# Kernel tuning notes

Measured on AMD Instinct MI355X. Metric: run time of the kernel, lower is better.

The kernel has to match this reference:

```python
import jax, jax.numpy as jnp
import numpy as np

TEMPERATURE = 0.5
BATCH_SIZE = 4096
EPS = 1e-8  # torch.nn.CosineSimilarity default eps


def setup_inputs() -> dict:
    key = jax.random.key(0)
    k1, k2 = jax.random.split(key)
    z1 = jax.random.normal(k1, (BATCH_SIZE, 256), dtype=jnp.float32)
    z2 = jax.random.normal(k2, (BATCH_SIZE, 256), dtype=jnp.float32)
    return {"z1": z1, "z2": z2}


def reference(z1, z2):
    B = z1.shape[0]
    N = 2 * B
    reps = jnp.concatenate([z1, z2], axis=0)  # [N, D]
    # Cosine similarity (torch clamps each norm to eps before dividing)
    norms = jnp.maximum(jnp.linalg.norm(reps, axis=1, keepdims=True), EPS)
    z = reps / norms
    sim = z @ z.T  # [N, N] cosine similarity matrix

    # positives: diagonals at offsets +B and -B (they are identical by symmetry,
    # but keep the original concat order: [diag(+B), diag(-B)])
    l_pos = jnp.diagonal(sim, offset=B)
    r_pos = jnp.diagonal(sim, offset=-B)
    positives = jnp.concatenate([l_pos, r_pos])  # [N]

    inv_t = 1.0 / TEMPERATURE
    pos_logit = positives * inv_t  # logits[:, 0]

    # negatives are all off-diagonal entries of each row (the positive pair is
    # thus present twice in the logits, faithful to the original). CE with
    # label 0 => loss_i = logsumexp(logits_i) - logits_i[0].
    neg_logits = jnp.where(jnp.eye(N, dtype=bool), -jnp.inf, sim * inv_t)
    lse = jnp.logaddexp(pos_logit, jax.scipy.special.logsumexp(neg_logits, axis=1))
    loss = jnp.sum(lse - pos_logit) / N
    return loss
```

## Files before the change

### kernel.cpp

```cpp
#include <hip/hip_runtime.h>
#include <hip/hip_bf16.h>
#include <cstdint>
#include <cstddef>
#include <math.h>

#define BSZ   4096
#define NROW  8192
#define DIM   256
#define INV_T 2.0f
#define EPS_N 1e-8f
#define CE    2.8853900817779268f
#define NTILE 2080

typedef __attribute__((ext_vector_type(8))) short bf16x8;
typedef __attribute__((ext_vector_type(4))) float f32x4;

struct TileOrder {
    unsigned short idx[NTILE];
    constexpr TileOrder() : idx{} {
        int pga[28] = {}, pgb[28] = {};
        int np = 0;
        for (int a = 0; a < 8; ++a)
            for (int b = a + 1; b < 8; ++b) { pga[np] = a; pgb[np] = b; ++np; }
        int seq[8][260] = {};
        for (int x = 0; x < 8; ++x) {
            int n = 0;
            for (int i = 0; i < 8; ++i)
                for (int j = i; j < 8; ++j)
                    seq[x][n++] = ((8 * x + i) << 8) | (8 * x + j);
            for (int p = 0; p < 3; ++p) {
                const int ga = pga[3 * x + p], gb = pgb[3 * x + p];
                for (int i = 0; i < 8; ++i)
                    for (int j = 0; j < 8; ++j)
                        seq[x][n++] = ((8 * ga + i) << 8) | (8 * gb + j);
            }
            const int pi = 24 + x / 2;
            const int ga = pga[pi], gb = pgb[pi];
            const int i0 = (x & 1) ? 4 : 0;
            for (int i = i0; i < i0 + 4; ++i)
                for (int j = 0; j < 8; ++j)
                    seq[x][n++] = ((8 * ga + i) << 8) | (8 * gb + j);
        }
        for (int l = 0; l < NTILE; ++l)
            idx[l] = (unsigned short)seq[l % 8][l / 8];
    }
};
__device__ constexpr TileOrder TO{};

__device__ __forceinline__ unsigned short f2bf(float x) {
    __hip_bfloat16 h = __float2bfloat16(x);
    return __builtin_bit_cast(unsigned short, h);
}
__device__ __forceinline__ float bf2f(unsigned short u) {
    __hip_bfloat16 h = __builtin_bit_cast(__hip_bfloat16, u);
    return __bfloat162float(h);
}

__device__ __forceinline__ void load_lds16(const void* g, void* l) {
    __builtin_amdgcn_global_load_lds(
        (const __attribute__((address_space(1))) void*)g,
        (__attribute__((address_space(3))) void*)l,
        16, 0, 0);
}

__global__ __launch_bounds__(256)
void nt_normalize(const float* __restrict__ z1,
                  const float* __restrict__ z2,
                  __hip_bfloat16* __restrict__ zn,
                  float* __restrict__ rowsum,
                  float* __restrict__ sii) {
    const int wave = threadIdx.x >> 6;
    const int lane = threadIdx.x & 63;
    const int row  = blockIdx.x * 4 + wave;
    const float* src = (row < BSZ) ? (z1 + (size_t)row * DIM)
                                   : (z2 + (size_t)(row - BSZ) * DIM);
    const float4 v = ((const float4*)src)[lane];
    float ss = v.x * v.x + v.y * v.y + v.z * v.z + v.w * v.w;
    #pragma unroll
    for (int off = 32; off; off >>= 1) ss += __shfl_xor(ss, off);
    const float rinv = 1.0f / fmaxf(sqrtf(ss), EPS_N);
    ushort4 o;
    o.x = f2bf(v.x * rinv);
    o.y = f2bf(v.y * rinv);
    o.z = f2bf(v.z * rinv);
    o.w = f2bf(v.w * rinv);
    ((ushort4*)(zn + (size_t)row * DIM))[lane] = o;
    float bx = bf2f(o.x), by = bf2f(o.y), bz = bf2f(o.z), bw = bf2f(o.w);
    float s2 = bx * bx + by * by + bz * bz + bw * bw;
    #pragma unroll
    for (int off = 32; off; off >>= 1) s2 += __shfl_xor(s2, off);
    if (lane == 0) { sii[row] = s2; rowsum[row] = 0.0f; }
}

__global__ __launch_bounds__(256)
void nt_gram(const __hip_bfloat16* __restrict__ zn,
             float* __restrict__ rowsum,
             float* __restrict__ pos) {
    const int code = TO.idx[blockIdx.x];
    const int bi = code >> 8, bj = code & 255;

    __shared__ __hip_bfloat16 As[128 * 64];
    __shared__ __hip_bfloat16 Bs[128 * 64];

    const int t    = threadIdx.x;
    const int lane = t & 63;
    const int wave = t >> 6;
    const int wrow = (wave >> 1) * 64;
    const int wcol = (wave & 1) * 64;
    const int q    = lane >> 4;
    const int r16  = lane & 15;
    const int sw   = r16 & 7;

    f32x4 acc[4][4] = {};

    const __hip_bfloat16* Ag = zn + (size_t)bi * 128 * DIM;
    const __hip_bfloat16* Bg = zn + (size_t)bj * 128 * DIM;

    const int srow = t >> 3;
    const int sc   = (t & 7) ^ (srow & 7);

    for (int k0 = 0; k0 < DIM; k0 += 64) {
        #pragma unroll
        for (int p = 0; p < 4; ++p) {
            const int row = p * 32 + srow;
            load_lds16(Ag + (size_t)row * DIM + k0 + sc * 8,
                       (char*)As + p * 4096 + t * 16);
            load_lds16(Bg + (size_t)row * DIM + k0 + sc * 8,
                       (char*)Bs + p * 4096 + t * 16);
        }
        __syncthreads();

        #pragma unroll
        for (int kk = 0; kk < 64; kk += 32) {
            const int cc = (kk >> 3) + q;
            const int cpos = (cc ^ sw) << 4;
            bf16x8 af[4], bfr[4];
            #pragma unroll
            for (int mi = 0; mi < 4; ++mi) {
                const int m = wrow + mi * 16 + r16;
                af[mi] = *(const bf16x8*)((const char*)As + m * 128 + cpos);
            }
            #pragma unroll
            for (int ni = 0; ni < 4; ++ni) {
                const int n = wcol + ni * 16 + r16;
                bfr[ni] = *(const bf16x8*)((const char*)Bs + n * 128 + cpos);
            }
            #pragma unroll
            for (int mi = 0; mi < 4; ++mi)
                #pragma unroll
                for (int ni = 0; ni < 4; ++ni)
                    acc[mi][ni] = __builtin_amdgcn_mfma_f32_16x16x32_bf16(
                        af[mi], bfr[ni], acc[mi][ni], 0, 0, 0);
        }
        __syncthreads();
    }

    const int c = lane & 15;
    float colp[4] = {0.f, 0.f, 0.f, 0.f};

    #pragma unroll
    for (int mi = 0; mi < 4; ++mi) {
        #pragma unroll
        for (int r = 0; r < 4; ++r) {
            float s = 0.f;
            #pragma unroll
            for (int ni = 0; ni < 4; ++ni) {
                const float e = exp2f(acc[mi][ni][r] * CE);
                s += e;
                colp[ni] += e;
            }
            s += __shfl_xor(s, 1);
            s += __shfl_xor(s, 2);
            s += __shfl_xor(s, 4);
            s += __shfl_xor(s, 8);
            if (c == 0) {
                const int grow = bi * 128 + wrow + mi * 16 + q * 4 + r;
                atomicAdd(&rowsum[grow], s);
            }
        }
    }
    if (bi != bj) {
        #pragma unroll
        for (int ni = 0; ni < 4; ++ni) {
            float cs = colp[ni];
            cs += __shfl_xor(cs, 16);
            cs += __shfl_xor(cs, 32);
            if (q == 0) atomicAdd(&rowsum[bj * 128 + wcol + ni * 16 + c], cs);
        }
    }
    if (bj == bi + 32 && wrow == wcol) {
        #pragma unroll
        for (int mi = 0; mi < 4; ++mi)
            #pragma unroll
            for (int r = 0; r < 4; ++r)
                if (c == q * 4 + r) {
                    const int grow = bi * 128 + wrow + mi * 16 + q * 4 + r;
                    const float val = acc[mi][mi][r];
                    pos[grow] = val;
                    pos[grow + BSZ] = val;
                }
    }
}

__global__ __launch_bounds__(1024)
void nt_finalize(const float* __restrict__ rowsum,
                 const float* __restrict__ pos,
                 const float* __restrict__ sii,
                 float* __restrict__ out) {
    float v = 0.f;
    for (int i = threadIdx.x; i < NROW; i += 1024) {
        const float pl  = pos[i] * INV_T;
        const float neg = rowsum[i] - exp2f(sii[i] * CE);
        v += logf(__expf(pl) + neg) - pl;
    }
    #pragma unroll
    for (int off = 32; off; off >>= 1) v += __shfl_xor(v, off);
    __shared__ float red[16];
    if ((threadIdx.x & 63) == 0) red[threadIdx.x >> 6] = v;
    __syncthreads();
    if (threadIdx.x == 0) {
        float s = 0.f;
        #pragma unroll
        for (int w = 0; w < 16; ++w) s += red[w];
        out[0] = s * (1.0f / NROW);
    }
}

extern "C" void kernel_launch(void* const* d_in, const int* in_sizes, int n_in,
                              void* d_out, int out_size, void* d_ws, size_t ws_size,
                              hipStream_t stream) {
    const float* z1 = (const float*)d_in[0];
    const float* z2 = (const float*)d_in[1];
    float* out = (float*)d_out;

    __hip_bfloat16* zn = (__hip_bfloat16*)d_ws;
    float* rowsum = (float*)((char*)d_ws + (size_t)NROW * DIM * 2);
    float* pos    = rowsum + NROW;
    float* sii    = pos + NROW;

    nt_normalize<<<NROW / 4, 256, 0, stream>>>(z1, z2, zn, rowsum, sii);
    nt_gram<<<NTILE, 256, 0, stream>>>(zn, rowsum, pos);
    nt_finalize<<<1, 1024, 0, stream>>>(rowsum, pos, sii, out);
}
```

Before: 107.0 us.

## Use 8-wave gram tiles with full-K A staging and split B prefetch

The gram kernel now runs 512 threads (8 waves in a 2x4 grid, each computing 64x32) instead of 4 waves each computing 64x64. The A tile is loaded for all 256 columns of K at once. B is loaded in two halves, and the second half is fetched while the first is being multiplied, replacing the four-stage load/sync loop with a single overlap step. This cuts barriers and raises the number of waves per tile to hide latency. In exchange, LDS use grows to 128KB per block, which likely limits occupancy to one block per CU.

```diff
diff --git a/kernel.cpp b/kernel.cpp
--- a/kernel.cpp
+++ b/kernel.cpp
@@ -92,113 +92,127 @@
     if (lane == 0) { sii[row] = s2; rowsum[row] = 0.0f; }
 }
 
-__global__ __launch_bounds__(256)
+__global__ __launch_bounds__(512)
 void nt_gram(const __hip_bfloat16* __restrict__ zn,
              float* __restrict__ rowsum,
              float* __restrict__ pos) {
     const int code = TO.idx[blockIdx.x];
     const int bi = code >> 8, bj = code & 255;
 
-    __shared__ __hip_bfloat16 As[128 * 64];
-    __shared__ __hip_bfloat16 Bs[128 * 64];
+    __shared__ __hip_bfloat16 As[128 * 256];
+    __shared__ __hip_bfloat16 Bs[2][128 * 128];
 
     const int t    = threadIdx.x;
     const int lane = t & 63;
     const int wave = t >> 6;
-    const int wrow = (wave >> 1) * 64;
-    const int wcol = (wave & 1) * 64;
+    const int wm   = wave >> 2;
+    const int wn   = wave & 3;
     const int q    = lane >> 4;
     const int r16  = lane & 15;
-    const int sw   = r16 & 7;
-
-    f32x4 acc[4][4] = {};
 
     const __hip_bfloat16* Ag = zn + (size_t)bi * 128 * DIM;
     const __hip_bfloat16* Bg = zn + (size_t)bj * 128 * DIM;
 
-    const int srow = t >> 3;
-    const int sc   = (t & 7) ^ (srow & 7);
-
-    for (int k0 = 0; k0 < DIM; k0 += 64) {
-        #pragma unroll
-        for (int p = 0; p < 4; ++p) {
-            const int row = p * 32 + srow;
-            load_lds16(Ag + (size_t)row * DIM + k0 + sc * 8,
-                       (char*)As + p * 4096 + t * 16);
-            load_lds16(Bg + (size_t)row * DIM + k0 + sc * 8,
-                       (char*)Bs + p * 4096 + t * 16);
-        }
-        __syncthreads();
-
-        #pragma unroll
-        for (int kk = 0; kk < 64; kk += 32) {
-            const int cc = (kk >> 3) + q;
-            const int cpos = (cc ^ sw) << 4;
-            bf16x8 af[4], bfr[4];
+    const int srowA = t >> 5, slotA = t & 31;
+    const int chA   = slotA ^ (srowA & 7);
+    const int srowB = t >> 4, slotB = t & 15;
+    const int chB   = slotB ^ (srowB & 7);
+
+    #pragma unroll
+    for (int p = 0; p < 8; ++p)
+        load_lds16(Ag + (size_t)(p * 16 + srowA) * DIM + chA * 8,
+                   (char*)As + p * 8192 + t * 16);
+    #pragma unroll
+    for (int p = 0; p < 4; ++p)
+        load_lds16(Bg + (size_t)(p * 32 + srowB) * DIM + chB * 8,
+                   (char*)Bs[0] + p * 8192 + t * 16);
+    __syncthreads();
+    #pragma unroll
+    for (int p = 0; p < 4; ++p)
+        load_lds16(Bg + (size_t)(p * 32 + srowB) * DIM + 128 + chB * 8,
+                   (char*)Bs[1] + p * 8192 + t * 16);
+
+    f32x4 acc[4][2] = {};
+
+    #pragma unroll
+    for (int h = 0; h < 2; ++h) {
+        if (h == 1) __syncthreads();
+        #pragma unroll
+        for (int kkl = 0; kkl < 4; ++kkl) {
+            const int ccA = (h * 4 + kkl) * 4 + q;
+            const int ccB = kkl * 4 + q;
+            bf16x8 af[4], bfr[2];
             #pragma unroll
             for (int mi = 0; mi < 4; ++mi) {
-                const int m = wrow + mi * 16 + r16;
-                af[mi] = *(const bf16x8*)((const char*)As + m * 128 + cpos);
+                const int m = wm * 64 + mi * 16 + r16;
+                af[mi] = *(const bf16x8*)((const char*)As + m * 512 +
+                                          ((ccA ^ (m & 7)) << 4));
             }
             #pragma unroll
-            for (int ni = 0; ni < 4; ++ni) {
-                const int n = wcol + ni * 16 + r16;
-                bfr[ni] = *(const bf16x8*)((const char*)Bs + n * 128 + cpos);
+            for (int ni = 0; ni < 2; ++ni) {
+                const int n = wn * 32 + ni * 16 + r16;
+                bfr[ni] = *(const bf16x8*)((const char*)Bs[h] + n * 256 +
+                                           ((ccB ^ (n & 7)) << 4));
             }
             #pragma unroll
             for (int mi = 0; mi < 4; ++mi)
                 #pragma unroll
-                for (int ni = 0; ni < 4; ++ni)
+                for (int ni = 0; ni < 2; ++ni)
                     acc[mi][ni] = __builtin_amdgcn_mfma_f32_16x16x32_bf16(
                         af[mi], bfr[ni], acc[mi][ni], 0, 0, 0);
         }
-        __syncthreads();
-    }
-
-    const int c = lane & 15;
-    float colp[4] = {0.f, 0.f, 0.f, 0.f};
+    }
+
+    const int c = r16;
+    f32x4 ev[4][2];
+    #pragma unroll
+    for (int mi = 0; mi < 4; ++mi)
+        #pragma unroll
+        for (int ni = 0; ni < 2; ++ni)
+            #pragma unroll
+            for (int r = 0; r < 4; ++r)
+                ev[mi][ni][r] = exp2f(acc[mi][ni][r] * CE);
 
     #pragma unroll
     for (int mi = 0; mi < 4; ++mi) {
-        #pragma unroll
-        for (int r = 0; r < 4; ++r) {
-            float s = 0.f;
-            #pragma unroll
-            for (int ni = 0; ni < 4; ++ni) {
-                const float e = exp2f(acc[mi][ni][r] * CE);
-                s += e;
-                colp[ni] += e;
-            }
-            s += __shfl_xor(s, 1);
-            s += __shfl_xor(s, 2);
-            s += __shfl_xor(s, 4);
-            s += __shfl_xor(s, 8);
-            if (c == 0) {
-                const int grow = bi * 128 + wrow + mi * 16 + q * 4 + r;
-                atomicAdd(&rowsum[grow], s);
-            }
+        f32x4 rv = ev[mi][0] + ev[mi][1];
+        #pragma unroll
+        for (int off = 1; off <= 8; off <<= 1)
+            #pragma unroll
+            for (int r = 0; r < 4; ++r)
+                rv[r] += __shfl_xor(rv[r], off);
+        if (c == 0) {
+            const int g0 = bi * 128 + wm * 64 + mi * 16 + q * 4;
+            atomicAdd(&rowsum[g0 + 0], rv[0]);
+            atomicAdd(&rowsum[g0 + 1], rv[1]);
+            atomicAdd(&rowsum[g0 + 2], rv[2]);
+            atomicAdd(&rowsum[g0 + 3], rv[3]);
         }
     }
     if (bi != bj) {
         #pragma unroll
-        for (int ni = 0; ni < 4; ++ni) {
-            float cs = colp[ni];
+        for (int ni = 0; ni < 2; ++ni) {
+            f32x4 cv = ev[0][ni] + ev[1][ni] + ev[2][ni] + ev[3][ni];
+            float cs = cv[0] + cv[1] + cv[2] + cv[3];
             cs += __shfl_xor(cs, 16);
             cs += __shfl_xor(cs, 32);
-            if (q == 0) atomicAdd(&rowsum[bj * 128 + wcol + ni * 16 + c], cs);
-        }
-    }
-    if (bj == bi + 32 && wrow == wcol) {
-        #pragma unroll
-        for (int mi = 0; mi < 4; ++mi)
+            if (q == 0)
+                atomicAdd(&rowsum[bj * 128 + wn * 32 + ni * 16 + c], cs);
+        }
+    }
+    if (bj == bi + 32 && wm == (wn >> 1)) {
+        #pragma unroll
+        for (int ni = 0; ni < 2; ++ni) {
+            const int mi = (wn & 1) * 2 + ni;
             #pragma unroll
             for (int r = 0; r < 4; ++r)
                 if (c == q * 4 + r) {
-                    const int grow = bi * 128 + wrow + mi * 16 + q * 4 + r;
-                    const float val = acc[mi][mi][r];
+                    const int grow = bi * 128 + wm * 64 + mi * 16 + q * 4 + r;
+                    const float val = acc[mi][ni][r];
                     pos[grow] = val;
                     pos[grow + BSZ] = val;
                 }
+        }
     }
 }
 
@@ -239,6 +253,6 @@
     float* sii    = pos + NROW;
 
     nt_normalize<<<NROW / 4, 256, 0, stream>>>(z1, z2, zn, rowsum, sii);
-    nt_gram<<<NTILE, 256, 0, stream>>>(zn, rowsum, pos);
+    nt_gram<<<NTILE, 512, 0, stream>>>(zn, rowsum, pos);
     nt_finalize<<<1, 1024, 0, stream>>>(rowsum, pos, sii, out);
 }
```

After: 249.6 us. +133.1%, slower.

## Make gram kernel persistent over four tiles with double-buffered LDS prefetch

Applied to the files above, without the earlier changes.

The gram kernel now launches 520 blocks, each processing four consecutive upper-triangle tiles. The K-chunk loads go into a double-buffered LDS ring so the next chunk, including the next tile's first chunk, is fetched while the current one is multiplied. The L2-friendly grouped tile order is replaced with plain row-major order, and launch bounds request two blocks per CU. This aims to hide global-load latency and cut per-block launch overhead, but doubles LDS use and may lose cache locality from the old ordering.

```diff
diff --git a/kernel.cpp b/kernel.cpp
--- a/kernel.cpp
+++ b/kernel.cpp
@@ -11,6 +11,7 @@
 #define EPS_N 1e-8f
 #define CE    2.8853900817779268f
 #define NTILE 2080
+#define GRID  520
 
 typedef __attribute__((ext_vector_type(8))) short bf16x8;
 typedef __attribute__((ext_vector_type(4))) float f32x4;
@@ -18,31 +19,10 @@
 struct TileOrder {
     unsigned short idx[NTILE];
     constexpr TileOrder() : idx{} {
-        int pga[28] = {}, pgb[28] = {};
-        int np = 0;
-        for (int a = 0; a < 8; ++a)
-            for (int b = a + 1; b < 8; ++b) { pga[np] = a; pgb[np] = b; ++np; }
-        int seq[8][260] = {};
-        for (int x = 0; x < 8; ++x) {
-            int n = 0;
-            for (int i = 0; i < 8; ++i)
-                for (int j = i; j < 8; ++j)
-                    seq[x][n++] = ((8 * x + i) << 8) | (8 * x + j);
-            for (int p = 0; p < 3; ++p) {
-                const int ga = pga[3 * x + p], gb = pgb[3 * x + p];
-                for (int i = 0; i < 8; ++i)
-                    for (int j = 0; j < 8; ++j)
-                        seq[x][n++] = ((8 * ga + i) << 8) | (8 * gb + j);
-            }
-            const int pi = 24 + x / 2;
-            const int ga = pga[pi], gb = pgb[pi];
-            const int i0 = (x & 1) ? 4 : 0;
-            for (int i = i0; i < i0 + 4; ++i)
-                for (int j = 0; j < 8; ++j)
-                    seq[x][n++] = ((8 * ga + i) << 8) | (8 * gb + j);
-        }
-        for (int l = 0; l < NTILE; ++l)
-            idx[l] = (unsigned short)seq[l % 8][l / 8];
+        int n = 0;
+        for (int bi = 0; bi < 64; ++bi)
+            for (int bj = bi; bj < 64; ++bj)
+                idx[n++] = (unsigned short)((bi << 8) | bj);
     }
 };
 __device__ constexpr TileOrder TO{};
@@ -92,15 +72,11 @@
     if (lane == 0) { sii[row] = s2; rowsum[row] = 0.0f; }
 }
 
-__global__ __launch_bounds__(256)
+__global__ __launch_bounds__(256, 2)
 void nt_gram(const __hip_bfloat16* __restrict__ zn,
              float* __restrict__ rowsum,
              float* __restrict__ pos) {
-    const int code = TO.idx[blockIdx.x];
-    const int bi = code >> 8, bj = code & 255;
-
-    __shared__ __hip_bfloat16 As[128 * 64];
-    __shared__ __hip_bfloat16 Bs[128 * 64];
+    __shared__ __hip_bfloat16 smem[2][2][128 * 64];
 
     const int t    = threadIdx.x;
     const int lane = t & 63;
@@ -111,94 +87,115 @@
     const int r16  = lane & 15;
     const int sw   = r16 & 7;
 
-    f32x4 acc[4][4] = {};
-
-    const __hip_bfloat16* Ag = zn + (size_t)bi * 128 * DIM;
-    const __hip_bfloat16* Bg = zn + (size_t)bj * 128 * DIM;
-
     const int srow = t >> 3;
     const int sc   = (t & 7) ^ (srow & 7);
 
-    for (int k0 = 0; k0 < DIM; k0 += 64) {
+    int codes[4];
+    #pragma unroll
+    for (int u = 0; u < 4; ++u) codes[u] = TO.idx[blockIdx.x * 4 + u];
+
+    auto issue = [&](int code, int kc, int par) {
+        const __hip_bfloat16* Ag = zn + (size_t)(code >> 8) * 128 * DIM + kc * 64;
+        const __hip_bfloat16* Bg = zn + (size_t)(code & 255) * 128 * DIM + kc * 64;
         #pragma unroll
         for (int p = 0; p < 4; ++p) {
             const int row = p * 32 + srow;
-            load_lds16(Ag + (size_t)row * DIM + k0 + sc * 8,
-                       (char*)As + p * 4096 + t * 16);
-            load_lds16(Bg + (size_t)row * DIM + k0 + sc * 8,
-                       (char*)Bs + p * 4096 + t * 16);
-        }
-        __syncthreads();
-
-        #pragma unroll
-        for (int kk = 0; kk < 64; kk += 32) {
-            const int cc = (kk >> 3) + q;
-            const int cpos = (cc ^ sw) << 4;
-            bf16x8 af[4], bfr[4];
-            #pragma unroll
-            for (int mi = 0; mi < 4; ++mi) {
-                const int m = wrow + mi * 16 + r16;
-                af[mi] = *(const bf16x8*)((const char*)As + m * 128 + cpos);
+            load_lds16(Ag + (size_t)row * DIM + sc * 8,
+                       (char*)smem[par][0] + p * 4096 + t * 16);
+            load_lds16(Bg + (size_t)row * DIM + sc * 8,
+                       (char*)smem[par][1] + p * 4096 + t * 16);
+        }
+    };
+
+    f32x4 acc[4][4] = {};
+    issue(codes[0], 0, 0);
+
+    for (int u = 0; u < 4; ++u) {
+        const int code = codes[u];
+        const int bi = code >> 8, bj = code & 255;
+
+        #pragma unroll
+        for (int kc = 0; kc < 4; ++kc) {
+            __syncthreads();
+            const int s = u * 4 + kc;
+            if (s + 1 < 16)
+                issue(codes[(s + 1) >> 2], (s + 1) & 3, (kc + 1) & 1);
+
+            const char* As = (const char*)smem[kc & 1][0];
+            const char* Bs = (const char*)smem[kc & 1][1];
+            #pragma unroll
+            for (int kk = 0; kk < 64; kk += 32) {
+                const int cc = (kk >> 3) + q;
+                const int cpos = (cc ^ sw) << 4;
+                bf16x8 af[4], bfr[4];
+                #pragma unroll
+                for (int mi = 0; mi < 4; ++mi) {
+                    const int m = wrow + mi * 16 + r16;
+                    af[mi] = *(const bf16x8*)(As + m * 128 + cpos);
+                }
+                #pragma unroll
+                for (int ni = 0; ni < 4; ++ni) {
+                    const int n = wcol + ni * 16 + r16;
+                    bfr[ni] = *(const bf16x8*)(Bs + n * 128 + cpos);
+                }
+                #pragma unroll
+                for (int mi = 0; mi < 4; ++mi)
+                    #pragma unroll
+                    for (int ni = 0; ni < 4; ++ni)
+                        acc[mi][ni] = __builtin_amdgcn_mfma_f32_16x16x32_bf16(
+                            af[mi], bfr[ni], acc[mi][ni], 0, 0, 0);
             }
+        }
+
+        const int c = r16;
+        float colp[4] = {0.f, 0.f, 0.f, 0.f};
+        #pragma unroll
+        for (int mi = 0; mi < 4; ++mi) {
+            #pragma unroll
+            for (int r = 0; r < 4; ++r) {
+                float s = 0.f;
+                #pragma unroll
+                for (int ni = 0; ni < 4; ++ni) {
+                    const float e = exp2f(acc[mi][ni][r] * CE);
+                    s += e;
+                    colp[ni] += e;
+                }
+                s += __shfl_xor(s, 1);
+                s += __shfl_xor(s, 2);
+                s += __shfl_xor(s, 4);
+                s += __shfl_xor(s, 8);
+                if (c == 0) {
+                    const int grow = bi * 128 + wrow + mi * 16 + q * 4 + r;
+                    atomicAdd(&rowsum[grow], s);
+                }
+            }
+        }
+        if (bi != bj) {
             #pragma unroll
             for (int ni = 0; ni < 4; ++ni) {
-                const int n = wcol + ni * 16 + r16;
-                bfr[ni] = *(const bf16x8*)((const char*)Bs + n * 128 + cpos);
+                float cs = colp[ni];
+                cs += __shfl_xor(cs, 16);
+                cs += __shfl_xor(cs, 32);
+                if (q == 0) atomicAdd(&rowsum[bj * 128 + wcol + ni * 16 + c], cs);
             }
+        }
+        if (bj == bi + 32 && wrow == wcol) {
             #pragma unroll
             for (int mi = 0; mi < 4; ++mi)
                 #pragma unroll
-                for (int ni = 0; ni < 4; ++ni)
-                    acc[mi][ni] = __builtin_amdgcn_mfma_f32_16x16x32_bf16(
-                        af[mi], bfr[ni], acc[mi][ni], 0, 0, 0);
-        }
-        __syncthreads();
-    }
-
-    const int c = lane & 15;
-    float colp[4] = {0.f, 0.f, 0.f, 0.f};
-
-    #pragma unroll
-    for (int mi = 0; mi < 4; ++mi) {
-        #pragma unroll
-        for (int r = 0; r < 4; ++r) {
-            float s = 0.f;
-            #pragma unroll
-            for (int ni = 0; ni < 4; ++ni) {
-                const float e = exp2f(acc[mi][ni][r] * CE);
-                s += e;
-                colp[ni] += e;
-            }
-            s += __shfl_xor(s, 1);
-            s += __shfl_xor(s, 2);
-            s += __shfl_xor(s, 4);
-            s += __shfl_xor(s, 8);
-            if (c == 0) {
-                const int grow = bi * 128 + wrow + mi * 16 + q * 4 + r;
-                atomicAdd(&rowsum[grow], s);
-            }
-        }
-    }
-    if (bi != bj) {
-        #pragma unroll
-        for (int ni = 0; ni < 4; ++ni) {
-            float cs = colp[ni];
-            cs += __shfl_xor(cs, 16);
-            cs += __shfl_xor(cs, 32);
-            if (q == 0) atomicAdd(&rowsum[bj * 128 + wcol + ni * 16 + c], cs);
-        }
-    }
-    if (bj == bi + 32 && wrow == wcol) {
+                for (int r = 0; r < 4; ++r)
+                    if (c == q * 4 + r) {
+                        const int grow = bi * 128 + wrow + mi * 16 + q * 4 + r;
+                        const float val = acc[mi][mi][r];
+                        pos[grow] = val;
+                        pos[grow + BSZ] = val;
+                    }
+        }
         #pragma unroll
         for (int mi = 0; mi < 4; ++mi)
             #pragma unroll
-            for (int r = 0; r < 4; ++r)
-                if (c == q * 4 + r) {
-                    const int grow = bi * 128 + wrow + mi * 16 + q * 4 + r;
-                    const float val = acc[mi][mi][r];
-                    pos[grow] = val;
-                    pos[grow + BSZ] = val;
-                }
+            for (int ni = 0; ni < 4; ++ni)
+                acc[mi][ni] = f32x4{0.f, 0.f, 0.f, 0.f};
     }
 }
 
@@ -239,6 +236,6 @@
     float* sii    = pos + NROW;
 
     nt_normalize<<<NROW / 4, 256, 0, stream>>>(z1, z2, zn, rowsum, sii);
-    nt_gram<<<NTILE, 256, 0, stream>>>(zn, rowsum, pos);
+    nt_gram<<<GRID, 256, 0, stream>>>(zn, rowsum, pos);
     nt_finalize<<<1, 1024, 0, stream>>>(rowsum, pos, sii, out);
 }
```

After: 120.4 us. 12.5% more time.
